# Performance work log

Measured on AMD Instinct MI355X. Metric: run time of the kernel, lower is better.

Reference implementation:

```python
import jax, jax.numpy as jnp
import numpy as np

L, N, E, H = 2048, 4, 2048, 16
D = E // H  # head_dim = 128
SCALE = D ** -0.5
NEG = -10000.0


def setup_inputs() -> dict:
    key = jax.random.key(0)
    ks = jax.random.split(key, 10)
    s = 0.02
    return {
        "query": jax.random.normal(ks[0], (L, N, E), jnp.float32),
        "key": jax.random.normal(ks[1], (L, N, E), jnp.float32),
        "wq": jax.random.normal(ks[2], (E, E), jnp.float32) * s,
        "wq_bias": jax.random.normal(ks[3], (E,), jnp.float32) * s,
        "wk": jax.random.normal(ks[4], (E, E), jnp.float32) * s,
        "wk_bias": jax.random.normal(ks[5], (E,), jnp.float32) * s,
        "wv": jax.random.normal(ks[6], (E, E), jnp.float32) * s,
        "wv_bias": jax.random.normal(ks[7], (E,), jnp.float32) * s,
        "wout": jax.random.normal(ks[8], (E, E), jnp.float32) * s,
        "wout_bias": jax.random.normal(ks[9], (E,), jnp.float32) * s,
    }


def reference(query, key, wq, wq_bias, wk, wk_bias, wv, wv_bias, wout, wout_bias):
    # query/key: (L, N, E). Projections: y = x @ W^T + b  (W: [inner, E])
    q = query @ wq.T + wq_bias          # (L, N, E)
    k = key @ wk.T + wk_bias
    v = key @ wv.T + wv_bias
    # split heads -> (N, H, L, D)
    def split(x):
        return x.reshape(L, N, H, D).transpose(1, 2, 0, 3)
    q, k, v = split(q) * SCALE, split(k), split(v)
    # scores (N, H, L, L) with causal mask (tril), fill -10000 like torch code
    attn = jnp.einsum("nhqd,nhkd->nhqk", q, k)
    causal = jnp.tril(jnp.ones((L, L), dtype=bool))
    attn = jnp.where(causal[None, None], attn, NEG)
    attn = jax.nn.softmax(attn, axis=-1)
    out = jnp.einsum("nhqk,nhkd->nhqd", attn, v)  # (N, H, L, D)
    out = out.transpose(2, 0, 1, 3).reshape(L, N, E)
    return out @ wout.T + wout_bias
```

## Files before the change

### kernel.cpp

```cpp
#include <hip/hip_runtime.h>
#include <hip/hip_bf16.h>
#include <cstdint>
#include <cstddef>

typedef __attribute__((ext_vector_type(8))) short short8;
typedef __attribute__((ext_vector_type(4))) float float4v;

#define L_SEQ 2048
#define N_B   4
#define E_DIM 2048
#define N_H   16
#define H_D   128
#define C1_SCALE_LOG2E 0.12751744f

static __device__ __forceinline__ unsigned short f2bf(float f) {
  union { float f; unsigned int u; } x; x.f = f;
  unsigned int u = x.u;
  u = u + 0x7fffu + ((u >> 16) & 1u);
  return (unsigned short)(u >> 16);
}

static __device__ __forceinline__ void g2l16(const void* g, void* l) {
  __builtin_amdgcn_global_load_lds(
      (const __attribute__((address_space(1))) unsigned int*)g,
      (__attribute__((address_space(3))) unsigned int*)l, 16, 0, 0);
}

__global__ __launch_bounds__(256) void cvt_kernel(const float* __restrict__ in,
                                                  unsigned short* __restrict__ out,
                                                  int n8) {
  int i = blockIdx.x * blockDim.x + threadIdx.x;
  if (i >= n8) return;
  const float4* p = (const float4*)in;
  float4 a = p[2 * i];
  float4 b = p[2 * i + 1];
  short8 o;
  o[0] = (short)f2bf(a.x); o[1] = (short)f2bf(a.y);
  o[2] = (short)f2bf(a.z); o[3] = (short)f2bf(a.w);
  o[4] = (short)f2bf(b.x); o[5] = (short)f2bf(b.y);
  o[6] = (short)f2bf(b.z); o[7] = (short)f2bf(b.w);
  *(short8*)(out + 8 * (size_t)i) = o;
}

#define BARC()                                         \
  do {                                                 \
    __builtin_amdgcn_s_barrier();                      \
    asm volatile("" ::: "memory");                     \
  } while (0)

#define STAGE(MAT, KT, KS, SLOT)                                          \
  do {                                                                    \
    g2l16((MAT) + (size_t)soff[0] + (size_t)((KT) * 128 + (KS) * 64),     \
          (char*)lds + (SLOT) * 16384 + lbase[0]);                        \
    g2l16((MAT) + (size_t)soff[1] + (size_t)((KT) * 128 + (KS) * 64),     \
          (char*)lds + (SLOT) * 16384 + lbase[1]);                        \
  } while (0)

template <int MODE>
__global__ __launch_bounds__(512) void gemm256(const unsigned short* __restrict__ A,
                                               const unsigned short* __restrict__ B,
                                               const float* __restrict__ bias,
                                               void* __restrict__ Cout) {
  __shared__ unsigned short lds[8][8192];
  const int tid = threadIdx.x;
  const int wid = tid >> 6, ln = tid & 63;
  const int wm = wid >> 2, wn = wid & 3;
  const int lhi = ln >> 4, llo = ln & 15;

  const int lin = (int)blockIdx.x;
  const int xcd = lin & 7, sl = lin >> 3;
  const int n0 = (sl & 7) * 256;
  const int m0 = (xcd * 4 + (sl >> 3)) * 256;

  const char* Apan = (const char*)(A + (size_t)m0 * E_DIM);
  const char* Bpan = (const char*)(B + (size_t)n0 * E_DIM);

  int soff[2], lbase[2];
#pragma unroll
  for (int i = 0; i < 2; ++i) {
    const int g = i * 512 + wid * 64 + ln;
    const int row = g >> 2, c = g & 3;
    soff[i] = row * (E_DIM * 2) + ((c ^ (row & 3)) << 4);
    lbase[i] = (i * 512 + wid * 64) * 16;
  }

  float4v acc[8][4] = {};
  const int arow = wm * 128 + llo;
  const int brow = wn * 64 + llo;
  const int swz = (lhi ^ (llo & 3)) * 8;
  constexpr int NT = E_DIM / 64;

  STAGE(Apan, 0, 0, 0); STAGE(Apan, 0, 1, 1);
  STAGE(Bpan, 0, 0, 2); STAGE(Bpan, 0, 1, 3);
  STAGE(Bpan, 1, 0, 6); STAGE(Apan, 1, 0, 4); STAGE(Bpan, 1, 1, 7);
  asm volatile("s_waitcnt vmcnt(6)" ::: "memory");
  BARC();

  short8 av[4], bv[4];
  for (int kt = 0; kt < NT; ++kt) {
    const int bb = kt & 1, ob = bb ^ 1;
    const unsigned short* pA = lds[bb * 4 + 0];
    const unsigned short* pB = lds[bb * 4 + 2];

#pragma unroll
    for (int mr = 0; mr < 4; ++mr)
      av[mr] = *(const short8*)(pA + (arow + mr * 16) * 32 + swz);
#pragma unroll
    for (int nr = 0; nr < 4; ++nr)
      bv[nr] = *(const short8*)(pB + (brow + nr * 16) * 32 + swz);
    if (kt + 1 < NT) STAGE(Apan, kt + 1, 1, ob * 4 + 1);
    BARC();
    __builtin_amdgcn_s_setprio(1);
#pragma unroll
    for (int mr = 0; mr < 4; ++mr)
#pragma unroll
      for (int nr = 0; nr < 4; ++nr)
        acc[mr][nr] = __builtin_amdgcn_mfma_f32_16x16x32_bf16(av[mr], bv[nr], acc[mr][nr], 0, 0, 0);
    __builtin_amdgcn_s_setprio(0);
    BARC();

#pragma unroll
    for (int mr = 0; mr < 4; ++mr)
      av[mr] = *(const short8*)(pA + (arow + 64 + mr * 16) * 32 + swz);
    if (kt + 2 < NT) STAGE(Bpan, kt + 2, 0, bb * 4 + 2);
    BARC();
    __builtin_amdgcn_s_setprio(1);
#pragma unroll
    for (int mr = 0; mr < 4; ++mr)
#pragma unroll
      for (int nr = 0; nr < 4; ++nr)
        acc[4 + mr][nr] = __builtin_amdgcn_mfma_f32_16x16x32_bf16(av[mr], bv[nr], acc[4 + mr][nr], 0, 0, 0);
    __builtin_amdgcn_s_setprio(0);
    BARC();

#pragma unroll
    for (int mr = 0; mr < 4; ++mr)
      av[mr] = *(const short8*)(pA + 8192 + (arow + mr * 16) * 32 + swz);
#pragma unroll
    for (int nr = 0; nr < 4; ++nr)
      bv[nr] = *(const short8*)(pB + 8192 + (brow + nr * 16) * 32 + swz);
    if (kt + 2 < NT) STAGE(Apan, kt + 2, 0, bb * 4 + 0);
    BARC();
    __builtin_amdgcn_s_setprio(1);
#pragma unroll
    for (int mr = 0; mr < 4; ++mr)
#pragma unroll
      for (int nr = 0; nr < 4; ++nr)
        acc[mr][nr] = __builtin_amdgcn_mfma_f32_16x16x32_bf16(av[mr], bv[nr], acc[mr][nr], 0, 0, 0);
    __builtin_amdgcn_s_setprio(0);
    BARC();

#pragma unroll
    for (int mr = 0; mr < 4; ++mr)
      av[mr] = *(const short8*)(pA + 8192 + (arow + 64 + mr * 16) * 32 + swz);
    if (kt + 2 < NT) STAGE(Bpan, kt + 2, 1, bb * 4 + 3);
    BARC();
    __builtin_amdgcn_s_setprio(1);
#pragma unroll
    for (int mr = 0; mr < 4; ++mr)
#pragma unroll
      for (int nr = 0; nr < 4; ++nr)
        acc[4 + mr][nr] = __builtin_amdgcn_mfma_f32_16x16x32_bf16(av[mr], bv[nr], acc[4 + mr][nr], 0, 0, 0);
    __builtin_amdgcn_s_setprio(0);

    if (kt < NT - 1) {
      if (kt == NT - 2) { asm volatile("s_waitcnt vmcnt(0)" ::: "memory"); }
      else              { asm volatile("s_waitcnt vmcnt(6)" ::: "memory"); }
      BARC();
    }
  }

  float bcol[4];
#pragma unroll
  for (int nr = 0; nr < 4; ++nr) bcol[nr] = bias[n0 + wn * 64 + nr * 16 + llo];

#pragma unroll
  for (int mr = 0; mr < 8; ++mr) {
#pragma unroll
    for (int r = 0; r < 4; ++r) {
      const int m = m0 + wm * 128 + mr * 16 + lhi * 4 + r;
      const int l = m >> 2, nb = m & 3;
#pragma unroll
      for (int nr = 0; nr < 4; ++nr) {
        const int cN = n0 + wn * 64 + nr * 16 + llo;
        const float v = acc[mr][nr][r] + bcol[nr];
        if (MODE == 0) {
          ((float*)Cout)[(size_t)m * E_DIM + cN] = v;
        } else if (MODE == 1) {
          const int h = cN >> 7, d = cN & 127;
          ((unsigned short*)Cout)[(((size_t)(nb * N_H + h)) * L_SEQ + l) * H_D + d] = f2bf(v);
        } else {
          const int h = cN >> 7, d = cN & 127;
          ((unsigned short*)Cout)[(((size_t)(nb * N_H + h)) * H_D + d) * L_SEQ + l] = f2bf(v);
        }
      }
    }
  }
}

__global__ __launch_bounds__(512, 2) void flash_attn(const unsigned short* __restrict__ Q,
                                                     const unsigned short* __restrict__ K,
                                                     const unsigned short* __restrict__ VT,
                                                     unsigned short* __restrict__ Cc) {
  __shared__ unsigned short sK[128 * 128];
  __shared__ unsigned short sV[128 * 128];
  const int tid = threadIdx.x;
  const int wv = tid >> 6, ln = tid & 63;
  const int lhi = ln >> 4, llo = ln & 15;
  const int kr = lhi * 8;
  const int lin = (int)blockIdx.x;
  const int xcd = lin & 7, slot = lin >> 3;
  const int hgrp = slot >> 4, pos = slot & 15;
  const int tq = (hgrp & 1) ? (15 - pos) : pos;
  const int nh = hgrp * 8 + xcd;
  const size_t hoff = (size_t)nh * (L_SEQ * H_D);
  const unsigned short* Qp = Q + hoff;
  const char* Kb = (const char*)(K + hoff);
  const char* Vb = (const char*)(VT + hoff);

  short8 qf[4];
#pragma unroll
  for (int kk = 0; kk < 4; ++kk)
    qf[kk] = *(const short8*)(Qp + (size_t)(tq * 128 + wv * 16 + llo) * H_D + kk * 32 + kr);

  float4v o_acc[8] = {};
  float mst[4], lst[4];
#pragma unroll
  for (int r = 0; r < 4; ++r) { mst[r] = -1e30f; lst[r] = 0.f; }

  for (int j = 0; j <= tq; ++j) {
#pragma unroll
    for (int t = 0; t < 4; ++t) {
      const int row = wv * 16 + t * 4 + lhi;
      const int sc = llo ^ (row & 7);
      g2l16(Kb + ((size_t)(j * 128 + row) * H_D) * 2 + sc * 16,
            (char*)sK + wv * 4096 + t * 1024);
      g2l16(Vb + ((size_t)row * L_SEQ + j * 128) * 2 + sc * 16,
            (char*)sV + wv * 4096 + t * 1024);
    }
    __syncthreads();

    float4v s[8] = {};
#pragma unroll
    for (int kk = 0; kk < 4; ++kk) {
      const int u0 = kk * 4 + lhi;
#pragma unroll
      for (int jj = 0; jj < 8; ++jj) {
        const int row = jj * 16 + llo;
        const short8 b = *(const short8*)(sK + row * 128 + (u0 ^ (row & 7)) * 8);
        s[jj] = __builtin_amdgcn_mfma_f32_16x16x32_bf16(qf[kk], b, s[jj], 0, 0, 0);
      }
    }

#pragma unroll
    for (int jj = 0; jj < 8; ++jj)
#pragma unroll
      for (int r = 0; r < 4; ++r)
        s[jj][r] *= C1_SCALE_LOG2E;
    const bool diag = (j == tq);
    if (diag) {
      const int qrow = wv * 16 + lhi * 4;
#pragma unroll
      for (int jj = 0; jj < 8; ++jj) {
        const int c = jj * 16 + llo;
#pragma unroll
        for (int r = 0; r < 4; ++r)
          if (c > qrow + r) s[jj][r] = -1e30f;
      }
    }

    float alpha[4];
#pragma unroll
    for (int r = 0; r < 4; ++r) {
      float rm = fmaxf(fmaxf(fmaxf(s[0][r], s[1][r]), fmaxf(s[2][r], s[3][r])),
                       fmaxf(fmaxf(s[4][r], s[5][r]), fmaxf(s[6][r], s[7][r])));
      rm = fmaxf(rm, __shfl_xor(rm, 1, 64));
      rm = fmaxf(rm, __shfl_xor(rm, 2, 64));
      rm = fmaxf(rm, __shfl_xor(rm, 4, 64));
      rm = fmaxf(rm, __shfl_xor(rm, 8, 64));
      const float mnew = fmaxf(mst[r], rm);
      const float a = __builtin_exp2f(mst[r] - mnew);
      mst[r] = mnew;
      alpha[r] = a;
      float rs = 0.f;
#pragma unroll
      for (int jj = 0; jj < 8; ++jj) {
        const float pv = __builtin_exp2f(s[jj][r] - mnew);
        s[jj][r] = pv;
        rs += pv;
      }
      rs += __shfl_xor(rs, 1, 64);
      rs += __shfl_xor(rs, 2, 64);
      rs += __shfl_xor(rs, 4, 64);
      rs += __shfl_xor(rs, 8, 64);
      lst[r] = lst[r] * a + rs;
    }

    __syncthreads();

#pragma unroll
    for (int r = 0; r < 4; ++r) {
      const int rl = wv * 16 + lhi * 4 + r;
#pragma unroll
      for (int jj = 0; jj < 8; ++jj) {
        const int c = jj * 16 + llo;
        const float v = s[jj][r];
        const float v2 = __shfl_xor(v, 1, 64);
        if ((llo & 1) == 0) {
          const unsigned int pk = (unsigned int)f2bf(v) | ((unsigned int)f2bf(v2) << 16);
          const int u = ((c >> 3) ^ (rl & 7));
          *(unsigned int*)(sK + rl * 128 + u * 8 + (c & 7)) = pk;
        }
      }
    }

#pragma unroll
    for (int jj = 0; jj < 8; ++jj) {
      float4v t = o_acc[jj];
      t[0] *= alpha[0]; t[1] *= alpha[1];
      t[2] *= alpha[2]; t[3] *= alpha[3];
      o_acc[jj] = t;
    }
#pragma unroll
    for (int kk = 0; kk < 4; ++kk) {
      const int u0 = kk * 4 + lhi;
      const int rowp = wv * 16 + llo;
      const short8 a = *(const short8*)(sK + rowp * 128 + (u0 ^ (rowp & 7)) * 8);
#pragma unroll
      for (int jj = 0; jj < 8; ++jj) {
        const int row = jj * 16 + llo;
        const short8 b = *(const short8*)(sV + row * 128 + (u0 ^ (row & 7)) * 8);
        o_acc[jj] = __builtin_amdgcn_mfma_f32_16x16x32_bf16(a, b, o_acc[jj], 0, 0, 0);
      }
    }
    __syncthreads();
  }

  const int nb = nh >> 4, h = nh & 15;
#pragma unroll
  for (int r = 0; r < 4; ++r) {
    const float inv = 1.0f / lst[r];
    const int rl = wv * 16 + lhi * 4 + r;
#pragma unroll
    for (int jj = 0; jj < 8; ++jj) {
      const int c = jj * 16 + llo;
      const float v = o_acc[jj][r] * inv;
      const float v2 = __shfl_xor(v, 1, 64);
      if ((llo & 1) == 0) {
        const unsigned int pk = (unsigned int)f2bf(v) | ((unsigned int)f2bf(v2) << 16);
        *(unsigned int*)(sK + rl * 128 + c) = pk;
      }
    }
  }
  __syncthreads();
#pragma unroll
  for (int t = 0; t < 4; ++t) {
    const int row = wv * 16 + t * 4 + lhi;
    const short8 val = *(const short8*)(sK + row * 128 + llo * 8);
    const int qg = tq * 128 + row;
    *(short8*)(Cc + ((size_t)qg * N_B + nb) * E_DIM + h * H_D + llo * 8) = val;
  }
}

extern "C" void kernel_launch(void* const* d_in, const int* in_sizes, int n_in,
                              void* d_out, int out_size, void* d_ws, size_t ws_size,
                              hipStream_t stream) {
  (void)in_sizes; (void)n_in; (void)out_size; (void)ws_size;
  const float* query = (const float*)d_in[0];
  const float* key   = (const float*)d_in[1];
  const float* wq = (const float*)d_in[2];
  const float* bq = (const float*)d_in[3];
  const float* wk = (const float*)d_in[4];
  const float* bk = (const float*)d_in[5];
  const float* wv = (const float*)d_in[6];
  const float* bv = (const float*)d_in[7];
  const float* wo = (const float*)d_in[8];
  const float* bo = (const float*)d_in[9];

  char* ws = (char*)d_ws;
  unsigned short* Xq = (unsigned short*)(ws);
  unsigned short* Xk = (unsigned short*)(ws + 33554432);
  unsigned short* Wq = (unsigned short*)(ws + 67108864);
  unsigned short* Wk = (unsigned short*)(ws + 75497472);
  unsigned short* Wv = (unsigned short*)(ws + 83886080);
  unsigned short* Wo = (unsigned short*)(ws + 92274688);
  unsigned short* Qh = (unsigned short*)(ws + 100663296);
  unsigned short* Kh = (unsigned short*)(ws + 134217728);
  unsigned short* VT = (unsigned short*)(ws + 167772160);
  unsigned short* Cc = Xq;

  const int nAct8 = L_SEQ * N_B * E_DIM / 8;
  const int nW8   = E_DIM * E_DIM / 8;
  cvt_kernel<<<dim3((nAct8 + 255) / 256), 256, 0, stream>>>(query, Xq, nAct8);
  cvt_kernel<<<dim3((nAct8 + 255) / 256), 256, 0, stream>>>(key, Xk, nAct8);
  cvt_kernel<<<dim3((nW8 + 255) / 256), 256, 0, stream>>>(wq, Wq, nW8);
  cvt_kernel<<<dim3((nW8 + 255) / 256), 256, 0, stream>>>(wk, Wk, nW8);
  cvt_kernel<<<dim3((nW8 + 255) / 256), 256, 0, stream>>>(wv, Wv, nW8);
  cvt_kernel<<<dim3((nW8 + 255) / 256), 256, 0, stream>>>(wo, Wo, nW8);

  dim3 gg(256);
  gemm256<1><<<gg, 512, 0, stream>>>(Xq, Wq, bq, Qh);
  gemm256<1><<<gg, 512, 0, stream>>>(Xk, Wk, bk, Kh);
  gemm256<2><<<gg, 512, 0, stream>>>(Xk, Wv, bv, VT);

  flash_attn<<<dim3(N_B * N_H * (L_SEQ / 128)), 512, 0, stream>>>(Qh, Kh, VT, Cc);

  gemm256<0><<<gg, 512, 0, stream>>>(Cc, Wo, bo, d_out);
}
```

Measured before the change: 817.0 us.

## Double-buffer K/V tiles in flash attention with 64-key blocks and async prefetch

```diff
diff --git a/kernel.cpp b/kernel.cpp
--- a/kernel.cpp
+++ b/kernel.cpp
@@ -25,6 +25,13 @@
       (const __attribute__((address_space(1))) unsigned int*)g,
       (__attribute__((address_space(3))) unsigned int*)l, 16, 0, 0);
 }
+
+#define BARF()                                          \
+  do {                                                  \
+    asm volatile("" ::: "memory");                      \
+    __builtin_amdgcn_s_barrier();                       \
+    asm volatile("" ::: "memory");                      \
+  } while (0)
 
 __global__ __launch_bounds__(256) void cvt_kernel(const float* __restrict__ in,
                                                   unsigned short* __restrict__ out,
@@ -198,12 +205,13 @@
   }
 }
 
-__global__ __launch_bounds__(512, 2) void flash_attn(const unsigned short* __restrict__ Q,
+__global__ __launch_bounds__(512, 4) void flash_attn(const unsigned short* __restrict__ Q,
                                                      const unsigned short* __restrict__ K,
                                                      const unsigned short* __restrict__ VT,
                                                      unsigned short* __restrict__ Cc) {
-  __shared__ unsigned short sK[128 * 128];
-  __shared__ unsigned short sV[128 * 128];
+  __shared__ unsigned short sK[2][64 * 128];
+  __shared__ unsigned short sV[2][128 * 64];
+  __shared__ unsigned short sP[128 * 64];
   const int tid = threadIdx.x;
   const int wv = tid >> 6, ln = tid & 63;
   const int lhi = ln >> 4, llo = ln & 15;
@@ -217,6 +225,7 @@
   const unsigned short* Qp = Q + hoff;
   const char* Kb = (const char*)(K + hoff);
   const char* Vb = (const char*)(VT + hoff);
+  const int jmax = 2 * tq + 1;
 
   short8 qf[4];
 #pragma unroll
@@ -228,41 +237,53 @@
 #pragma unroll
   for (int r = 0; r < 4; ++r) { mst[r] = -1e30f; lst[r] = 0.f; }
 
-  for (int j = 0; j <= tq; ++j) {
-#pragma unroll
-    for (int t = 0; t < 4; ++t) {
-      const int row = wv * 16 + t * 4 + lhi;
-      const int sc = llo ^ (row & 7);
-      g2l16(Kb + ((size_t)(j * 128 + row) * H_D) * 2 + sc * 16,
-            (char*)sK + wv * 4096 + t * 1024);
-      g2l16(Vb + ((size_t)row * L_SEQ + j * 128) * 2 + sc * 16,
-            (char*)sV + wv * 4096 + t * 1024);
-    }
-    __syncthreads();
-
-    float4v s[8] = {};
+#define STAGE_T(J, BUF)                                                     \
+  do {                                                                      \
+    _Pragma("unroll")                                                       \
+    for (int i = 0; i < 2; ++i) {                                           \
+      const int g = wv * 128 + i * 64 + ln;                                 \
+      const int rk = g >> 4, ck = g & 15;                                   \
+      g2l16(Kb + ((size_t)((J) * 64 + rk) * H_D) * 2 + (ck ^ (rk & 7)) * 16,\
+            (char*)sK[BUF] + wv * 2048 + i * 1024);                         \
+      const int rv = g >> 3, cv = g & 7;                                    \
+      g2l16(Vb + ((size_t)rv * L_SEQ + (J) * 64) * 2 + (cv ^ (rv & 7)) * 16,\
+            (char*)sV[BUF] + wv * 2048 + i * 1024);                         \
+    }                                                                       \
+  } while (0)
+
+  STAGE_T(0, 0);
+  STAGE_T(1, 1);
+  asm volatile("s_waitcnt vmcnt(4)" ::: "memory");
+  BARF();
+
+  for (int j = 0; j <= jmax; ++j) {
+    const int cur = j & 1;
+    const unsigned short* sKc = sK[cur];
+    const unsigned short* sVc = sV[cur];
+
+    float4v s[4] = {};
 #pragma unroll
     for (int kk = 0; kk < 4; ++kk) {
       const int u0 = kk * 4 + lhi;
 #pragma unroll
-      for (int jj = 0; jj < 8; ++jj) {
+      for (int jj = 0; jj < 4; ++jj) {
         const int row = jj * 16 + llo;
-        const short8 b = *(const short8*)(sK + row * 128 + (u0 ^ (row & 7)) * 8);
+        const short8 b = *(const short8*)(sKc + row * 128 + (u0 ^ (row & 7)) * 8);
         s[jj] = __builtin_amdgcn_mfma_f32_16x16x32_bf16(qf[kk], b, s[jj], 0, 0, 0);
       }
     }
 
 #pragma unroll
-    for (int jj = 0; jj < 8; ++jj)
+    for (int jj = 0; jj < 4; ++jj)
 #pragma unroll
       for (int r = 0; r < 4; ++r)
         s[jj][r] *= C1_SCALE_LOG2E;
-    const bool diag = (j == tq);
-    if (diag) {
+    if (j >= 2 * tq) {
+      const int off = (j - 2 * tq) * 64;
       const int qrow = wv * 16 + lhi * 4;
 #pragma unroll
-      for (int jj = 0; jj < 8; ++jj) {
-        const int c = jj * 16 + llo;
+      for (int jj = 0; jj < 4; ++jj) {
+        const int c = jj * 16 + llo + off;
 #pragma unroll
         for (int r = 0; r < 4; ++r)
           if (c > qrow + r) s[jj][r] = -1e30f;
@@ -272,8 +293,7 @@
     float alpha[4];
 #pragma unroll
     for (int r = 0; r < 4; ++r) {
-      float rm = fmaxf(fmaxf(fmaxf(s[0][r], s[1][r]), fmaxf(s[2][r], s[3][r])),
-                       fmaxf(fmaxf(s[4][r], s[5][r]), fmaxf(s[6][r], s[7][r])));
+      float rm = fmaxf(fmaxf(s[0][r], s[1][r]), fmaxf(s[2][r], s[3][r]));
       rm = fmaxf(rm, __shfl_xor(rm, 1, 64));
       rm = fmaxf(rm, __shfl_xor(rm, 2, 64));
       rm = fmaxf(rm, __shfl_xor(rm, 4, 64));
@@ -284,7 +304,7 @@
       alpha[r] = a;
       float rs = 0.f;
 #pragma unroll
-      for (int jj = 0; jj < 8; ++jj) {
+      for (int jj = 0; jj < 4; ++jj) {
         const float pv = __builtin_exp2f(s[jj][r] - mnew);
         s[jj][r] = pv;
         rs += pv;
@@ -296,20 +316,18 @@
       lst[r] = lst[r] * a + rs;
     }
 
-    __syncthreads();
-
 #pragma unroll
     for (int r = 0; r < 4; ++r) {
       const int rl = wv * 16 + lhi * 4 + r;
 #pragma unroll
-      for (int jj = 0; jj < 8; ++jj) {
+      for (int jj = 0; jj < 4; ++jj) {
         const int c = jj * 16 + llo;
         const float v = s[jj][r];
         const float v2 = __shfl_xor(v, 1, 64);
         if ((llo & 1) == 0) {
           const unsigned int pk = (unsigned int)f2bf(v) | ((unsigned int)f2bf(v2) << 16);
           const int u = ((c >> 3) ^ (rl & 7));
-          *(unsigned int*)(sK + rl * 128 + u * 8 + (c & 7)) = pk;
+          *(unsigned int*)(sP + rl * 64 + u * 8 + (c & 7)) = pk;
         }
       }
     }
@@ -321,21 +339,29 @@
       t[2] *= alpha[2]; t[3] *= alpha[3];
       o_acc[jj] = t;
     }
-#pragma unroll
-    for (int kk = 0; kk < 4; ++kk) {
+    const int rowp = wv * 16 + llo;
+#pragma unroll
+    for (int kk = 0; kk < 2; ++kk) {
       const int u0 = kk * 4 + lhi;
-      const int rowp = wv * 16 + llo;
-      const short8 a = *(const short8*)(sK + rowp * 128 + (u0 ^ (rowp & 7)) * 8);
+      const short8 a = *(const short8*)(sP + rowp * 64 + (u0 ^ (rowp & 7)) * 8);
 #pragma unroll
       for (int jj = 0; jj < 8; ++jj) {
         const int row = jj * 16 + llo;
-        const short8 b = *(const short8*)(sV + row * 128 + (u0 ^ (row & 7)) * 8);
+        const short8 b = *(const short8*)(sVc + row * 64 + (u0 ^ (row & 7)) * 8);
         o_acc[jj] = __builtin_amdgcn_mfma_f32_16x16x32_bf16(a, b, o_acc[jj], 0, 0, 0);
       }
     }
-    __syncthreads();
-  }
-
+
+    BARF();
+    if (j + 2 <= jmax) STAGE_T(j + 2, cur);
+    if (j + 1 <= jmax) {
+      if (j + 2 <= jmax) { asm volatile("s_waitcnt vmcnt(4)" ::: "memory"); }
+      else               { asm volatile("s_waitcnt vmcnt(0)" ::: "memory"); }
+      BARF();
+    }
+  }
+
+  unsigned short* sO = &sK[0][0];
   const int nb = nh >> 4, h = nh & 15;
 #pragma unroll
   for (int r = 0; r < 4; ++r) {
@@ -348,18 +374,19 @@
       const float v2 = __shfl_xor(v, 1, 64);
       if ((llo & 1) == 0) {
         const unsigned int pk = (unsigned int)f2bf(v) | ((unsigned int)f2bf(v2) << 16);
-        *(unsigned int*)(sK + rl * 128 + c) = pk;
-      }
-    }
-  }
-  __syncthreads();
+        *(unsigned int*)(sO + rl * 128 + c) = pk;
+      }
+    }
+  }
+  BARF();
 #pragma unroll
   for (int t = 0; t < 4; ++t) {
     const int row = wv * 16 + t * 4 + lhi;
-    const short8 val = *(const short8*)(sK + row * 128 + llo * 8);
+    const short8 val = *(const short8*)(sO + row * 128 + llo * 8);
     const int qg = tq * 128 + row;
     *(short8*)(Cc + ((size_t)qg * N_B + nb) * E_DIM + h * H_D + llo * 8) = val;
   }
+#undef STAGE_T
 }
 
 extern "C" void kernel_launch(void* const* d_in, const int* in_sizes, int n_in,
```

Result: no change. 822.4 us (+0.7%).
